# Optimization experiments

Hardware: AMD Instinct MI355X
Metric: run time of the kernel (lower is better)

The kernel has to match this reference:

```python
import jax, jax.numpy as jnp
import numpy as np

B, H, W, C, NH, WS, SS = 32, 56, 56, 192, 6, 7, 3
L = H * W
N = WS * WS
HD = C // NH
EPS = 1e-3  # keras LayerNormalization default epsilon


def _rel_index(ws):
    coords = np.stack(np.meshgrid(np.arange(ws), np.arange(ws), indexing='ij')).reshape(2, -1)
    rel = (coords[:, :, None] - coords[:, None, :]).transpose(1, 2, 0)
    rel[..., 0] += ws - 1
    rel[..., 1] += ws - 1
    rel[..., 0] *= 2 * ws - 1
    return rel.sum(-1)  # (N, N) int


def _attn_mask(h, w, ws, ss):
    img = np.zeros((h, w), np.float32)
    cnt = 0
    for hs in (slice(0, -ws), slice(-ws, -ss), slice(-ss, None)):
        for wsl in (slice(0, -ws), slice(-ws, -ss), slice(-ss, None)):
            img[hs, wsl] = cnt
            cnt += 1
    mw = img.reshape(h // ws, ws, w // ws, ws).transpose(0, 2, 1, 3).reshape(-1, ws * ws)
    diff = mw[:, None, :] - mw[:, :, None]  # expand_dims(mw,1) - expand_dims(mw,2)
    return np.where(diff != 0, -100.0, 0.0).astype(np.float32)  # (nW, N, N)


REL_IDX = _rel_index(WS)
ATTN_MASK = _attn_mask(H, W, WS, SS)


def _ln(x, g, b):
    m = x.mean(-1, keepdims=True)
    v = x.var(-1, keepdims=True)
    return (x - m) / jnp.sqrt(v + EPS) * g + b


def setup_inputs() -> dict:
    key = jax.random.key(0)
    ks = jax.random.split(key, 8)
    s = 0.02
    return {
        'x': jax.random.normal(ks[0], (B, L, C), jnp.float32),
        'gamma1': jnp.ones((C,), jnp.float32),
        'beta1': jnp.zeros((C,), jnp.float32),
        'qkv_w': jax.random.normal(ks[1], (C, 3 * C), jnp.float32) * s,
        'qkv_b': jnp.zeros((3 * C,), jnp.float32),
        'proj_w': jax.random.normal(ks[2], (C, C), jnp.float32) * s,
        'proj_b': jnp.zeros((C,), jnp.float32),
        'rel_bias_table': jax.random.normal(ks[3], ((2 * WS - 1) ** 2, NH), jnp.float32) * s,
        'gamma2': jnp.ones((C,), jnp.float32),
        'beta2': jnp.zeros((C,), jnp.float32),
        'fc1_w': jax.random.normal(ks[4], (C, 4 * C), jnp.float32) * s,
        'fc1_b': jnp.zeros((4 * C,), jnp.float32),
        'fc2_w': jax.random.normal(ks[5], (4 * C, C), jnp.float32) * s,
        'fc2_b': jnp.zeros((C,), jnp.float32),
    }


def reference(x, gamma1, beta1, qkv_w, qkv_b, proj_w, proj_b, rel_bias_table,
              gamma2, beta2, fc1_w, fc1_b, fc2_w, fc2_b):
    scale = HD ** -0.5
    shortcut = x
    # norm1 + cyclic shift + window partition
    xn = _ln(x, gamma1, beta1).reshape(B, H, W, C)
    xn = jnp.roll(xn, (-SS, -SS), axis=(1, 2))
    xw = xn.reshape(B, H // WS, WS, W // WS, WS, C).transpose(0, 1, 3, 2, 4, 5).reshape(-1, N, C)
    # window attention
    qkv = (xw @ qkv_w + qkv_b).reshape(-1, N, 3, NH, HD).transpose(2, 0, 3, 1, 4)
    q, k, v = qkv[0] * scale, qkv[1], qkv[2]  # (B*nW, NH, N, HD)
    attn = jnp.einsum('whnd,whmd->whnm', q, k)
    bias = rel_bias_table[REL_IDX.reshape(-1)].reshape(N, N, NH).transpose(2, 0, 1)
    attn = attn + bias[None]
    nW = ATTN_MASK.shape[0]
    attn = attn.reshape(B, nW, NH, N, N) + jnp.asarray(ATTN_MASK)[None, :, None]
    attn = jax.nn.softmax(attn.reshape(-1, NH, N, N), axis=-1)
    out = jnp.einsum('whnm,whmd->whnd', attn, v).transpose(0, 2, 1, 3).reshape(-1, N, C)
    out = out @ proj_w + proj_b
    # window reverse + reverse shift
    xr = out.reshape(B, H // WS, W // WS, WS, WS, C).transpose(0, 1, 3, 2, 4, 5).reshape(B, H, W, C)
    xr = jnp.roll(xr, (SS, SS), axis=(1, 2)).reshape(B, L, C)
    x = shortcut + xr
    # MLP block
    y = _ln(x, gamma2, beta2)
    y = jax.nn.gelu(y @ fc1_w + fc1_b, approximate=False) @ fc2_w + fc2_b
    return x + y
```

## Files before the change

### kernel.cpp

```cpp
#include <hip/hip_runtime.h>
#include <math.h>

namespace {
constexpr int kBatch = 32, kH = 56, kW = 56, kC = 192, kNH = 6, kWS = 7, kSS = 3;
constexpr int kL   = kH * kW;
constexpr int kN   = kWS * kWS;
constexpr int kTok = kBatch * kL;
constexpr int kNWin = kTok / kN;
constexpr float kEps   = 1e-3f;
constexpr float kScale = 0.17677669529663687f;
}

typedef unsigned short u16;
typedef __attribute__((ext_vector_type(8))) short short8;
typedef __attribute__((ext_vector_type(4))) float f32x4;

__device__ __forceinline__ float bf2f(u16 u) {
    return __uint_as_float(((unsigned int)u) << 16);
}
__device__ __forceinline__ u16 f2bf(float f) {
    unsigned int x = __float_as_uint(f);
    return (u16)((x + 0x7FFFu + ((x >> 16) & 1u)) >> 16);
}
__device__ __forceinline__ float gelu_f(float x) {
    float z = 0.7978845608028654f * x * (1.0f + 0.044715f * x * x);
    float t = 1.0f - 2.0f / (1.0f + __expf(2.0f * z));
    return 0.5f * x * (1.0f + t);
}

__global__ __launch_bounds__(256) void ln_kernel(
    const float* __restrict__ x, const float* __restrict__ gamma,
    const float* __restrict__ beta, u16* __restrict__ out, int do_shift)
{
    const int wave = threadIdx.x >> 6;
    const int lane = threadIdx.x & 63;
    const int tok = (blockIdx.x << 2) + wave;
    const float* xp = x + (size_t)tok * kC;
    float v0 = xp[lane], v1 = xp[lane + 64], v2 = xp[lane + 128];
    float s  = v0 + v1 + v2;
    float sq = v0 * v0 + v1 * v1 + v2 * v2;
    #pragma unroll
    for (int off = 32; off > 0; off >>= 1) {
        s  += __shfl_down(s, off, 64);
        sq += __shfl_down(sq, off, 64);
    }
    s  = __shfl(s, 0, 64);
    sq = __shfl(sq, 0, 64);
    const float mean = s * (1.0f / kC);
    const float var  = sq * (1.0f / kC) - mean * mean;
    const float inv  = rsqrtf(var + kEps);
    size_t orow;
    if (do_shift) {
        const int b = tok / kL, hw = tok % kL;
        const int h = hw / kW, w = hw % kW;
        const int hs = (h + kH - kSS) % kH;
        const int ws = (w + kW - kSS) % kW;
        const int wh = hs / kWS, ii = hs % kWS;
        const int ww = ws / kWS, jj = ws % kWS;
        orow = (size_t)(b * 64 + wh * 8 + ww) * kN + (ii * kWS + jj);
    } else {
        orow = tok;
    }
    u16* op = out + orow * kC;
    op[lane]       = f2bf((v0 - mean) * inv * gamma[lane]       + beta[lane]);
    op[lane + 64]  = f2bf((v1 - mean) * inv * gamma[lane + 64]  + beta[lane + 64]);
    op[lane + 128] = f2bf((v2 - mean) * inv * gamma[lane + 128] + beta[lane + 128]);
}

__global__ __launch_bounds__(256) void wprep_qkv(
    const float* __restrict__ w, u16* __restrict__ wt)
{
    const int idx = blockIdx.x * 256 + threadIdx.x;
    if (idx >= 576 * 192) return;
    const int n = idx / 192, k = idx - n * 192;
    float v = w[(size_t)k * 576 + n];
    if (n < 192) v *= kScale;
    wt[idx] = f2bf(v);
}

__global__ __launch_bounds__(256) void wprep_rest(
    const float* __restrict__ pw, const float* __restrict__ f1w,
    const float* __restrict__ f2w, u16* __restrict__ proj_t,
    u16* __restrict__ f1_t, u16* __restrict__ f2_t)
{
    int idx = blockIdx.x * 256 + threadIdx.x;
    if (idx < 36864) {
        const int n = idx / 192, k = idx - n * 192;
        proj_t[idx] = f2bf(pw[(size_t)k * 192 + n]);
        return;
    }
    idx -= 36864;
    if (idx < 147456) {
        const int n = idx / 192, k = idx - n * 192;
        f1_t[idx] = f2bf(f1w[(size_t)k * 768 + n]);
        return;
    }
    idx -= 147456;
    if (idx < 147456) {
        const int n = idx / 768, k = idx - n * 768;
        f2_t[idx] = f2bf(f2w[(size_t)k * 192 + n]);
    }
}

__global__ __launch_bounds__(256) void prep_bm(
    const float* __restrict__ btab, const float* __restrict__ qkv_b,
    float* __restrict__ T, float* __restrict__ qkv_bs)
{
    const int idx = blockIdx.x * 256 + threadIdx.x;
    if (idx < 576) qkv_bs[idx] = (idx < 192) ? qkv_b[idx] * kScale : qkv_b[idx];
    if (idx >= 4 * 6 * 49 * 49) return;
    const int m = idx % 49, n = (idx / 49) % 49;
    const int head = (idx / 2401) % 6, cls = idx / (2401 * 6);
    const int i1 = n / 7, j1 = n % 7, i2 = m / 7, j2 = m % 7;
    float v = btab[((i1 - i2 + 6) * 13 + (j1 - j2 + 6)) * kNH + head];
    const int whE = cls >> 1, wwE = cls & 1;
    const int r1 = (whE ? (i1 < 4 ? 1 : 2) : 0) * 3 + (wwE ? (j1 < 4 ? 1 : 2) : 0);
    const int r2 = (whE ? (i2 < 4 ? 1 : 2) : 0) * 3 + (wwE ? (j2 < 4 ? 1 : 2) : 0);
    if (r1 != r2) v -= 100.f;
    T[idx] = v;
}

template <int MODE, int K, int NJ>
__global__ __launch_bounds__(256) void gemm_mfma(
    const u16* __restrict__ A, const u16* __restrict__ Bt, int ldb,
    const float* __restrict__ bias, const float* __restrict__ aux,
    void* __restrict__ outv, u16* __restrict__ vt = nullptr)
{
    constexpr int Nn = NJ * 192;
    constexpr int Kp = K + 8;
    __shared__ u16 As[64 * Kp];
    const int tid  = threadIdx.x;
    const int wave = tid >> 6, lane = tid & 63;
    const int quad = lane >> 4, l15 = lane & 15;
    const int m0 = blockIdx.x * 64;

    {
        const u16* src = A + (size_t)m0 * K;
        #pragma unroll
        for (int i = tid; i < 64 * K / 8; i += 256) {
            const int e = i * 8;
            const int r = e / K, c = e - r * K;
            *(short8*)&As[r * Kp + c] = *(const short8*)(src + e);
        }
    }
    __syncthreads();

    #pragma unroll
    for (int j = 0; j < NJ; ++j) {
        const int nb0 = j * 192 + wave * 48;
        const u16* Bbase = Bt + (size_t)(nb0 + l15) * ldb + quad * 8;
        f32x4 acc[4][3] = {};
        #pragma unroll
        for (int ks = 0; ks < K / 32; ++ks) {
            short8 a[4], b[3];
            #pragma unroll
            for (int i = 0; i < 4; ++i)
                a[i] = *(const short8*)&As[(i * 16 + l15) * Kp + ks * 32 + quad * 8];
            #pragma unroll
            for (int t = 0; t < 3; ++t)
                b[t] = *(const short8*)(Bbase + (size_t)t * 16 * ldb + ks * 32);
            #pragma unroll
            for (int i = 0; i < 4; ++i)
                #pragma unroll
                for (int t = 0; t < 3; ++t)
                    acc[i][t] = __builtin_amdgcn_mfma_f32_16x16x32_bf16(
                        a[i], b[t], acc[i][t], 0, 0, 0);
        }
        float bcol[3] = {0.f, 0.f, 0.f};
        {
            #pragma unroll
            for (int t = 0; t < 3; ++t) bcol[t] = bias[nb0 + t * 16 + l15];
        }
        #pragma unroll
        for (int i = 0; i < 4; ++i) {
            #pragma unroll
            for (int reg = 0; reg < 4; ++reg) {
                const int r = m0 + i * 16 + quad * 4 + reg;
                if (MODE == 2) {
                    const int win = r / kN, n = r % kN;
                    const int b = win >> 6, wi = win & 63;
                    const int wh = wi >> 3, ww = wi & 7;
                    const int i1 = n / kWS, j1 = n % kWS;
                    const int h = (wh * kWS + i1 + kSS) % kH;
                    const int w = (ww * kWS + j1 + kSS) % kW;
                    const size_t drow = ((size_t)b * kL + h * kW + w) * kC;
                    #pragma unroll
                    for (int t = 0; t < 3; ++t) {
                        const int c = nb0 + t * 16 + l15;
                        const size_t dest = drow + c;
                        ((float*)outv)[dest] = acc[i][t][reg] + bcol[t] + aux[dest];
                    }
                } else if (MODE == 5 && j == 2) {
                    const int win = r / kN, n = r - win * kN;
                    #pragma unroll
                    for (int t = 0; t < 3; ++t) {
                        const int d = nb0 - 384 + t * 16 + l15;
                        const size_t off =
                            ((size_t)win * 192 + d) * 64 + n;
                        vt[off] = f2bf(acc[i][t][reg] + bcol[t]);
                    }
                } else {
                    #pragma unroll
                    for (int t = 0; t < 3; ++t) {
                        const int c = nb0 + t * 16 + l15;
                        float v = acc[i][t][reg] + bcol[t];
                        ((u16*)outv)[(size_t)r * Nn + c] = f2bf(v);
                    }
                }
            }
        }
    }
}

__global__ __launch_bounds__(256) void mlp_fused(
    float* __restrict__ out,
    const float* __restrict__ gamma, const float* __restrict__ beta,
    const u16* __restrict__ f1_t, const float* __restrict__ fc1_b,
    const u16* __restrict__ f2_t, const float* __restrict__ fc2_b)
{
    constexpr int Kp = 200;
    constexpr int Hp = 200;
    __shared__ u16 As[64 * Kp];
    __shared__ u16 Hs[64 * Hp];
    const int tid  = threadIdx.x;
    const int wave = tid >> 6, lane = tid & 63;
    const int quad = lane >> 4, l15 = lane & 15;
    const int m0 = blockIdx.x * 64;

    {
        float gv[12], bv[12];
        #pragma unroll
        for (int j = 0; j < 12; ++j) {
            gv[j] = gamma[l15 * 12 + j];
            bv[j] = beta[l15 * 12 + j];
        }
        #pragma unroll
        for (int it = 0; it < 4; ++it) {
            const int r = it * 16 + wave * 4 + quad;
            const float* xp = out + (size_t)(m0 + r) * kC + l15 * 12;
            float4 u0 = *(const float4*)(xp);
            float4 u1 = *(const float4*)(xp + 4);
            float4 u2 = *(const float4*)(xp + 8);
            float v[12] = {u0.x, u0.y, u0.z, u0.w, u1.x, u1.y, u1.z, u1.w,
                           u2.x, u2.y, u2.z, u2.w};
            float s = 0.f, sq = 0.f;
            #pragma unroll
            for (int j = 0; j < 12; ++j) { s += v[j]; sq += v[j] * v[j]; }
            #pragma unroll
            for (int off = 1; off < 16; off <<= 1) {
                s  += __shfl_xor(s, off, 64);
                sq += __shfl_xor(sq, off, 64);
            }
            const float mean = s * (1.0f / kC);
            const float inv  = rsqrtf(sq * (1.0f / kC) - mean * mean + kEps);
            unsigned* ap = (unsigned*)&As[r * Kp + l15 * 12];
            #pragma unroll
            for (int j = 0; j < 6; ++j) {
                float a0 = (v[2 * j]     - mean) * inv * gv[2 * j]     + bv[2 * j];
                float a1 = (v[2 * j + 1] - mean) * inv * gv[2 * j + 1] + bv[2 * j + 1];
                ap[j] = (unsigned)f2bf(a0) | ((unsigned)f2bf(a1) << 16);
            }
        }
    }
    __syncthreads();

    f32x4 acc2[4][3] = {};
    for (int c = 0; c < 4; ++c) {
        f32x4 acc1[4][3] = {};
        {
            const u16* B1 = f1_t + (size_t)(c * 192 + wave * 48 + l15) * 192 + quad * 8;
            #pragma unroll
            for (int ks = 0; ks < 6; ++ks) {
                short8 a[4], b[3];
                #pragma unroll
                for (int i = 0; i < 4; ++i)
                    a[i] = *(const short8*)&As[(i * 16 + l15) * Kp + ks * 32 + quad * 8];
                #pragma unroll
                for (int t = 0; t < 3; ++t)
                    b[t] = *(const short8*)(B1 + (size_t)t * 16 * 192 + ks * 32);
                #pragma unroll
                for (int i = 0; i < 4; ++i)
                    #pragma unroll
                    for (int t = 0; t < 3; ++t)
                        acc1[i][t] = __builtin_amdgcn_mfma_f32_16x16x32_bf16(
                            a[i], b[t], acc1[i][t], 0, 0, 0);
            }
        }
        __syncthreads();
        #pragma unroll
        for (int t = 0; t < 3; ++t) {
            const int cc = wave * 48 + t * 16 + l15;
            const float bb = fc1_b[c * 192 + cc];
            #pragma unroll
            for (int i = 0; i < 4; ++i) {
                #pragma unroll
                for (int reg = 0; reg < 4; ++reg) {
                    const int r = i * 16 + quad * 4 + reg;
                    Hs[r * Hp + cc] = f2bf(gelu_f(acc1[i][t][reg] + bb));
                }
            }
        }
        __syncthreads();
        {
            const u16* B2 = f2_t + (size_t)(wave * 48 + l15) * 768 + c * 192 + quad * 8;
            #pragma unroll
            for (int ks = 0; ks < 6; ++ks) {
                short8 a[4], b[3];
                #pragma unroll
                for (int i = 0; i < 4; ++i)
                    a[i] = *(const short8*)&Hs[(i * 16 + l15) * Hp + ks * 32 + quad * 8];
                #pragma unroll
                for (int t = 0; t < 3; ++t)
                    b[t] = *(const short8*)(B2 + (size_t)t * 16 * 768 + ks * 32);
                #pragma unroll
                for (int i = 0; i < 4; ++i)
                    #pragma unroll
                    for (int t = 0; t < 3; ++t)
                        acc2[i][t] = __builtin_amdgcn_mfma_f32_16x16x32_bf16(
                            a[i], b[t], acc2[i][t], 0, 0, 0);
            }
        }
    }
    #pragma unroll
    for (int t = 0; t < 3; ++t) {
        const int cc = wave * 48 + t * 16 + l15;
        const float bb = fc2_b[cc];
        #pragma unroll
        for (int i = 0; i < 4; ++i) {
            #pragma unroll
            for (int reg = 0; reg < 4; ++reg) {
                const int r = m0 + i * 16 + quad * 4 + reg;
                float* p = out + (size_t)r * kC + cc;
                *p = acc2[i][t][reg] + bb + *p;
            }
        }
    }
}

__global__ __launch_bounds__(256) void attn_mfma(
    const u16* __restrict__ qkv, const u16* __restrict__ vt,
    const float* __restrict__ T, u16* __restrict__ out)
{
    __shared__ u16 Ps[4][64][72];
    const int tid = threadIdx.x;
    const int wave = tid >> 6, lane = tid & 63;
    const int quad = lane >> 4, l15 = lane & 15;
    const int pair = blockIdx.x * 4 + wave;
    const int win = pair / 6, head = pair - win * 6;
    const int wi = win & 63;
    const int cls = (((wi >> 3) == 7) ? 2 : 0) + (((wi & 7) == 7) ? 1 : 0);
    const float* Tb = T + (size_t)(cls * 6 + head) * 49 * 49;

    const u16* base = qkv + (size_t)win * 49 * 576 + head * 32 + quad * 8;
    short8 zz = {};
    short8 qa[4], kb[4];
    #pragma unroll
    for (int i = 0; i < 4; ++i) {
        const int n = i * 16 + l15;
        qa[i] = (n < 49) ? *(const short8*)(base + (size_t)n * 576) : zz;
        kb[i] = (n < 49) ? *(const short8*)(base + (size_t)n * 576 + 192) : zz;
    }
    f32x4 acc[4][4];
    #pragma unroll
    for (int i = 0; i < 4; ++i) {
        #pragma unroll
        for (int reg = 0; reg < 4; ++reg) {
            const int n = i * 16 + quad * 4 + reg;
            const bool nv = (n < 49);
            const float* Trow = Tb + (nv ? n : 0) * 49;
            #pragma unroll
            for (int j = 0; j < 3; ++j)
                acc[i][j][reg] = nv ? Trow[j * 16 + l15] : 0.f;
            acc[i][3][reg] = (nv && l15 == 0) ? Trow[48] : -30000.f;
        }
    }
    #pragma unroll
    for (int i = 0; i < 4; ++i)
        #pragma unroll
        for (int j = 0; j < 4; ++j)
            acc[i][j] = __builtin_amdgcn_mfma_f32_16x16x32_bf16(
                qa[i], kb[j], acc[i][j], 0, 0, 0);
    float rowinv[4][4];
    #pragma unroll
    for (int i = 0; i < 4; ++i) {
        #pragma unroll
        for (int reg = 0; reg < 4; ++reg) {
            const int n = i * 16 + quad * 4 + reg;
            float e0 = __expf(acc[i][0][reg]), e1 = __expf(acc[i][1][reg]);
            float e2 = __expf(acc[i][2][reg]), e3 = __expf(acc[i][3][reg]);
            float sum = e0 + e1 + e2 + e3;
            #pragma unroll
            for (int off = 1; off < 16; off <<= 1)
                sum += __shfl_xor(sum, off, 64);
            rowinv[i][reg] = 1.0f / sum;
            Ps[wave][n][0 * 16 + l15] = f2bf(e0);
            Ps[wave][n][1 * 16 + l15] = f2bf(e1);
            Ps[wave][n][2 * 16 + l15] = f2bf(e2);
            Ps[wave][n][3 * 16 + l15] = f2bf(e3);
        }
    }
    const u16* vb_base = vt + ((size_t)pair * 32 + l15) * 64 + quad * 8;
    f32x4 o[4][2] = {};
    #pragma unroll
    for (int ks = 0; ks < 2; ++ks) {
        short8 pa[4], vb[2];
        #pragma unroll
        for (int i = 0; i < 4; ++i)
            pa[i] = *(const short8*)&Ps[wave][i * 16 + l15][ks * 32 + quad * 8];
        #pragma unroll
        for (int t = 0; t < 2; ++t)
            vb[t] = *(const short8*)(vb_base + (size_t)t * 16 * 64 + ks * 32);
        #pragma unroll
        for (int i = 0; i < 4; ++i)
            #pragma unroll
            for (int t = 0; t < 2; ++t)
                o[i][t] = __builtin_amdgcn_mfma_f32_16x16x32_bf16(
                    pa[i], vb[t], o[i][t], 0, 0, 0);
    }
    u16* obase = out + (size_t)win * 49 * 192 + head * 32;
    #pragma unroll
    for (int i = 0; i < 4; ++i) {
        #pragma unroll
        for (int reg = 0; reg < 4; ++reg) {
            const int n = i * 16 + quad * 4 + reg;
            if (n < 49) {
                const float inv = rowinv[i][reg];
                obase[(size_t)n * 192 + l15]      = f2bf(o[i][0][reg] * inv);
                obase[(size_t)n * 192 + 16 + l15] = f2bf(o[i][1][reg] * inv);
            }
        }
    }
}

extern "C" void kernel_launch(void* const* d_in, const int* in_sizes, int n_in,
                              void* d_out, int out_size, void* d_ws, size_t ws_size,
                              hipStream_t stream)
{
    const float* x      = (const float*)d_in[0];
    const float* gamma1 = (const float*)d_in[1];
    const float* beta1  = (const float*)d_in[2];
    const float* qkv_w  = (const float*)d_in[3];
    const float* qkv_b  = (const float*)d_in[4];
    const float* proj_w = (const float*)d_in[5];
    const float* proj_b = (const float*)d_in[6];
    const float* btab   = (const float*)d_in[7];
    const float* gamma2 = (const float*)d_in[8];
    const float* beta2  = (const float*)d_in[9];
    const float* fc1_w  = (const float*)d_in[10];
    const float* fc1_b  = (const float*)d_in[11];
    const float* fc2_w  = (const float*)d_in[12];
    const float* fc2_b  = (const float*)d_in[13];
    float* out = (float*)d_out;

    u16* buf_a = (u16*)d_ws;
    u16* buf_b = buf_a + (size_t)kTok * 192;
    u16* qkv_t = (u16*)d_out;
    float* bm_tab = (float*)d_out + 55296;
    float* qkv_bs = bm_tab + 57624;
    u16* vT = (u16*)d_out + 230400;
    u16* wt2   = (u16*)d_ws + (size_t)kTok * 768 - 331776;
    u16* proj_t = wt2;
    u16* f1_t   = wt2 + 36864;
    u16* f2_t   = f1_t + 147456;

    wprep_qkv<<<(110592 + 255) / 256, 256, 0, stream>>>(qkv_w, qkv_t);
    prep_bm<<<(57624 + 255) / 256, 256, 0, stream>>>(btab, qkv_b, bm_tab, qkv_bs);
    ln_kernel<<<kTok / 4, 256, 0, stream>>>(x, gamma1, beta1, buf_a, 1);
    gemm_mfma<5, 192, 3><<<kTok / 64, 256, 0, stream>>>(
        buf_a, qkv_t, 192, qkv_bs, nullptr, buf_b, vT);
    attn_mfma<<<(kNWin * kNH) / 4, 256, 0, stream>>>(buf_b, vT, bm_tab, buf_a);
    wprep_rest<<<(331776 + 255) / 256, 256, 0, stream>>>(
        proj_w, fc1_w, fc2_w, proj_t, f1_t, f2_t);
    gemm_mfma<2, 192, 1><<<kTok / 64, 256, 0, stream>>>(
        buf_a, proj_t, 192, proj_b, x, out);
    mlp_fused<<<kTok / 64, 256, 0, stream>>>(
        out, gamma2, beta2, f1_t, fc1_b, f2_t, fc2_b);
}
```

Measured before the change: 529.0 us.

## Fuse projection GEMM, residual, LayerNorm and MLP into one kernel via row map

Merges the output projection GEMM (with window-reverse, roll and residual add) into the MLP kernel. The post-attention residual stays in registers and LayerNorm statistics are reduced across waves through shared memory. This removes one full fp32 write and re-read of the intermediate activation, plus a kernel launch. A precomputed row-destination map replaces the per-element index arithmetic. In exchange the kernel gathers x rows in scattered order, needs more registers and adds two extra block-level barriers.

Result: faster. 498.1 us (-5.8%).

```diff
diff --git a/kernel.cpp b/kernel.cpp
--- a/kernel.cpp
+++ b/kernel.cpp
@@ -81,7 +81,7 @@
 __global__ __launch_bounds__(256) void wprep_rest(
     const float* __restrict__ pw, const float* __restrict__ f1w,
     const float* __restrict__ f2w, u16* __restrict__ proj_t,
-    u16* __restrict__ f1_t, u16* __restrict__ f2_t)
+    u16* __restrict__ f1_t, u16* __restrict__ f2_t, int* __restrict__ rowmap)
 {
     int idx = blockIdx.x * 256 + threadIdx.x;
     if (idx < 36864) {
@@ -99,6 +99,17 @@
     if (idx < 147456) {
         const int n = idx / 768, k = idx - n * 768;
         f2_t[idx] = f2bf(f2w[(size_t)k * 192 + n]);
+        return;
+    }
+    idx -= 147456;
+    if (idx < kTok) {
+        const int win = idx / kN, n = idx - win * kN;
+        const int b = win >> 6, wi = win & 63;
+        const int wh = wi >> 3, ww = wi & 7;
+        const int i1 = n / kWS, j1 = n - i1 * kWS;
+        const int h = (wh * kWS + i1 + kSS) % kH;
+        const int w = (ww * kWS + j1 + kSS) % kW;
+        rowmap[idx] = b * kL + h * kW + w;
     }
 }
 
@@ -176,21 +187,7 @@
             #pragma unroll
             for (int reg = 0; reg < 4; ++reg) {
                 const int r = m0 + i * 16 + quad * 4 + reg;
-                if (MODE == 2) {
-                    const int win = r / kN, n = r % kN;
-                    const int b = win >> 6, wi = win & 63;
-                    const int wh = wi >> 3, ww = wi & 7;
-                    const int i1 = n / kWS, j1 = n % kWS;
-                    const int h = (wh * kWS + i1 + kSS) % kH;
-                    const int w = (ww * kWS + j1 + kSS) % kW;
-                    const size_t drow = ((size_t)b * kL + h * kW + w) * kC;
-                    #pragma unroll
-                    for (int t = 0; t < 3; ++t) {
-                        const int c = nb0 + t * 16 + l15;
-                        const size_t dest = drow + c;
-                        ((float*)outv)[dest] = acc[i][t][reg] + bcol[t] + aux[dest];
-                    }
-                } else if (MODE == 5 && j == 2) {
+                if (MODE == 5 && j == 2) {
                     const int win = r / kN, n = r - win * kN;
                     #pragma unroll
                     for (int t = 0; t < 3; ++t) {
@@ -212,53 +209,132 @@
     }
 }
 
-__global__ __launch_bounds__(256) void mlp_fused(
-    float* __restrict__ out,
+__global__ __launch_bounds__(256) void proj_mlp_fused(
+    const u16* __restrict__ A,
+    const u16* __restrict__ proj_t, const float* __restrict__ proj_b,
+    const float* __restrict__ x,
+    const int* __restrict__ rowmap,
     const float* __restrict__ gamma, const float* __restrict__ beta,
     const u16* __restrict__ f1_t, const float* __restrict__ fc1_b,
-    const u16* __restrict__ f2_t, const float* __restrict__ fc2_b)
+    const u16* __restrict__ f2_t, const float* __restrict__ fc2_b,
+    float* __restrict__ out)
 {
     constexpr int Kp = 200;
     constexpr int Hp = 200;
     __shared__ u16 As[64 * Kp];
     __shared__ u16 Hs[64 * Hp];
+    __shared__ int rowdest[64];
     const int tid  = threadIdx.x;
     const int wave = tid >> 6, lane = tid & 63;
     const int quad = lane >> 4, l15 = lane & 15;
     const int m0 = blockIdx.x * 64;
+    float* Hsf = (float*)Hs;
 
     {
-        float gv[12], bv[12];
-        #pragma unroll
-        for (int j = 0; j < 12; ++j) {
-            gv[j] = gamma[l15 * 12 + j];
-            bv[j] = beta[l15 * 12 + j];
-        }
-        #pragma unroll
-        for (int it = 0; it < 4; ++it) {
-            const int r = it * 16 + wave * 4 + quad;
-            const float* xp = out + (size_t)(m0 + r) * kC + l15 * 12;
-            float4 u0 = *(const float4*)(xp);
-            float4 u1 = *(const float4*)(xp + 4);
-            float4 u2 = *(const float4*)(xp + 8);
-            float v[12] = {u0.x, u0.y, u0.z, u0.w, u1.x, u1.y, u1.z, u1.w,
-                           u2.x, u2.y, u2.z, u2.w};
-            float s = 0.f, sq = 0.f;
-            #pragma unroll
-            for (int j = 0; j < 12; ++j) { s += v[j]; sq += v[j] * v[j]; }
+        const u16* src = A + (size_t)m0 * 192;
+        #pragma unroll
+        for (int i = tid; i < 64 * 192 / 8; i += 256) {
+            const int e = i * 8;
+            const int r = e / 192, c = e - r * 192;
+            *(short8*)&As[r * Kp + c] = *(const short8*)(src + e);
+        }
+        if (tid < 64) rowdest[tid] = rowmap[m0 + tid];
+    }
+    __syncthreads();
+
+    float x1[4][3][4];
+    #pragma unroll
+    for (int i = 0; i < 4; ++i) {
+        #pragma unroll
+        for (int reg = 0; reg < 4; ++reg) {
+            const float* xr = x + (size_t)rowdest[i * 16 + quad * 4 + reg] * kC
+                              + wave * 48 + l15;
+            #pragma unroll
+            for (int t = 0; t < 3; ++t) x1[i][t][reg] = xr[t * 16];
+        }
+    }
+
+    f32x4 acc[4][3] = {};
+    {
+        const u16* Bbase = proj_t + (size_t)(wave * 48 + l15) * 192 + quad * 8;
+        #pragma unroll
+        for (int ks = 0; ks < 6; ++ks) {
+            short8 a[4], b[3];
+            #pragma unroll
+            for (int i = 0; i < 4; ++i)
+                a[i] = *(const short8*)&As[(i * 16 + l15) * Kp + ks * 32 + quad * 8];
+            #pragma unroll
+            for (int t = 0; t < 3; ++t)
+                b[t] = *(const short8*)(Bbase + (size_t)t * 16 * 192 + ks * 32);
+            #pragma unroll
+            for (int i = 0; i < 4; ++i)
+                #pragma unroll
+                for (int t = 0; t < 3; ++t)
+                    acc[i][t] = __builtin_amdgcn_mfma_f32_16x16x32_bf16(
+                        a[i], b[t], acc[i][t], 0, 0, 0);
+        }
+    }
+    {
+        float bcol[3];
+        #pragma unroll
+        for (int t = 0; t < 3; ++t) bcol[t] = proj_b[wave * 48 + t * 16 + l15];
+        #pragma unroll
+        for (int i = 0; i < 4; ++i)
+            #pragma unroll
+            for (int t = 0; t < 3; ++t)
+                #pragma unroll
+                for (int reg = 0; reg < 4; ++reg)
+                    x1[i][t][reg] += acc[i][t][reg] + bcol[t];
+    }
+
+    #pragma unroll
+    for (int i = 0; i < 4; ++i) {
+        #pragma unroll
+        for (int reg = 0; reg < 4; ++reg) {
+            float s  = x1[i][0][reg] + x1[i][1][reg] + x1[i][2][reg];
+            float sq = x1[i][0][reg] * x1[i][0][reg]
+                     + x1[i][1][reg] * x1[i][1][reg]
+                     + x1[i][2][reg] * x1[i][2][reg];
             #pragma unroll
             for (int off = 1; off < 16; off <<= 1) {
                 s  += __shfl_xor(s, off, 64);
                 sq += __shfl_xor(sq, off, 64);
             }
-            const float mean = s * (1.0f / kC);
-            const float inv  = rsqrtf(sq * (1.0f / kC) - mean * mean + kEps);
-            unsigned* ap = (unsigned*)&As[r * Kp + l15 * 12];
-            #pragma unroll
-            for (int j = 0; j < 6; ++j) {
-                float a0 = (v[2 * j]     - mean) * inv * gv[2 * j]     + bv[2 * j];
-                float a1 = (v[2 * j + 1] - mean) * inv * gv[2 * j + 1] + bv[2 * j + 1];
-                ap[j] = (unsigned)f2bf(a0) | ((unsigned)f2bf(a1) << 16);
+            if (l15 == 0) {
+                const int r = i * 16 + quad * 4 + reg;
+                Hsf[r * 8 + wave * 2]     = s;
+                Hsf[r * 8 + wave * 2 + 1] = sq;
+            }
+        }
+    }
+    __syncthreads();
+    if (tid < 64) {
+        const float s  = Hsf[tid * 8] + Hsf[tid * 8 + 2] + Hsf[tid * 8 + 4] + Hsf[tid * 8 + 6];
+        const float sq = Hsf[tid * 8 + 1] + Hsf[tid * 8 + 3] + Hsf[tid * 8 + 5] + Hsf[tid * 8 + 7];
+        const float mean = s * (1.0f / kC);
+        const float inv  = rsqrtf(sq * (1.0f / kC) - mean * mean + kEps);
+        Hsf[512 + tid * 2]     = mean;
+        Hsf[512 + tid * 2 + 1] = inv;
+    }
+    __syncthreads();
+    {
+        float gv[3], bv[3];
+        #pragma unroll
+        for (int t = 0; t < 3; ++t) {
+            gv[t] = gamma[wave * 48 + t * 16 + l15];
+            bv[t] = beta[wave * 48 + t * 16 + l15];
+        }
+        #pragma unroll
+        for (int i = 0; i < 4; ++i) {
+            #pragma unroll
+            for (int reg = 0; reg < 4; ++reg) {
+                const int r = i * 16 + quad * 4 + reg;
+                const float mean = Hsf[512 + r * 2];
+                const float inv  = Hsf[513 + r * 2];
+                #pragma unroll
+                for (int t = 0; t < 3; ++t)
+                    As[r * Kp + wave * 48 + t * 16 + l15] =
+                        f2bf((x1[i][t][reg] - mean) * inv * gv[t] + bv[t]);
             }
         }
     }
@@ -329,9 +405,8 @@
         for (int i = 0; i < 4; ++i) {
             #pragma unroll
             for (int reg = 0; reg < 4; ++reg) {
-                const int r = m0 + i * 16 + quad * 4 + reg;
-                float* p = out + (size_t)r * kC + cc;
-                *p = acc2[i][t][reg] + bb + *p;
+                const int dr = rowdest[i * 16 + quad * 4 + reg];
+                out[(size_t)dr * kC + cc] = x1[i][t][reg] + acc2[i][t][reg] + bb;
             }
         }
     }
@@ -462,6 +537,7 @@
     u16* proj_t = wt2;
     u16* f1_t   = wt2 + 36864;
     u16* f2_t   = f1_t + 147456;
+    int* rowmap = (int*)buf_b;
 
     wprep_qkv<<<(110592 + 255) / 256, 256, 0, stream>>>(qkv_w, qkv_t);
     prep_bm<<<(57624 + 255) / 256, 256, 0, stream>>>(btab, qkv_b, bm_tab, qkv_bs);
@@ -469,10 +545,9 @@
     gemm_mfma<5, 192, 3><<<kTok / 64, 256, 0, stream>>>(
         buf_a, qkv_t, 192, qkv_bs, nullptr, buf_b, vT);
     attn_mfma<<<(kNWin * kNH) / 4, 256, 0, stream>>>(buf_b, vT, bm_tab, buf_a);
-    wprep_rest<<<(331776 + 255) / 256, 256, 0, stream>>>(
-        proj_w, fc1_w, fc2_w, proj_t, f1_t, f2_t);
-    gemm_mfma<2, 192, 1><<<kTok / 64, 256, 0, stream>>>(
-        buf_a, proj_t, 192, proj_b, x, out);
-    mlp_fused<<<kTok / 64, 256, 0, stream>>>(
-        out, gamma2, beta2, f1_t, fc1_b, f2_t, fc2_b);
-}
+    wprep_rest<<<(331776 + kTok + 255) / 256, 256, 0, stream>>>(
+        proj_w, fc1_w, fc2_w, proj_t, f1_t, f2_t, rowmap);
+    proj_mlp_fused<<<kTok / 64, 256, 0, stream>>>(
+        buf_a, proj_t, proj_b, x, rowmap,
+        gamma2, beta2, f1_t, fc1_b, f2_t, fc2_b, out);
+}
```
